# Optimization experiments

Measured on AMD Instinct MI355X. Metric: run time of the kernel, lower is better.

## Reference

```python
import jax, jax.numpy as jnp
import numpy as np

N = 4096      # num_nodes
D_IN = 768    # input_dim
HID = 512     # hidden_dim per head
D_OUT = 768   # output_dim
H = 4         # num_heads
ALPHA = 0.2   # LeakyReLU slope
NEG_BIG = -9e15


def _layer_norm(x, g, b, eps=1e-5):
    m = jnp.mean(x, axis=-1, keepdims=True)
    v = jnp.var(x, axis=-1, keepdims=True)
    return (x - m) * jax.lax.rsqrt(v + eps) * g + b


def _multihead_gat(h, mask, ew, W, a, concat):
    # h: [N, F_in], W: [H, F_in, O], a: [H, 2*O], mask/ew: [N, N]
    O = W.shape[-1]
    Wh = jnp.einsum('nf,hfo->hno', h, W)                      # [H, N, O]
    # e[h,i,j] = leakyrelu(a1.Wh[i] + a2.Wh[j]) -- equivalent to the
    # concat(Wh_i, Wh_j) @ a formulation, without the O(N^2 * 2O) tensor.
    s_src = jnp.einsum('hno,ho->hn', Wh, a[:, :O])            # [H, N]
    s_dst = jnp.einsum('hno,ho->hn', Wh, a[:, O:])            # [H, N]
    e = jax.nn.leaky_relu(s_src[:, :, None] + s_dst[:, None, :], negative_slope=ALPHA)
    att = jnp.where(mask[None], e, NEG_BIG)
    if ew is not None:
        att = att * ew[None]                                   # faithful: scale AFTER masking
    att = jax.nn.softmax(att, axis=-1)                         # dropout is identity at eval
    hp = jnp.einsum('hnm,hmo->hno', att, Wh)                   # [H, N, O]
    if concat:
        return jax.nn.elu(jnp.transpose(hp, (1, 0, 2)).reshape(h.shape[0], H * O))
    return jnp.mean(hp, axis=0)                                # concat=False: mean, no ELU


def setup_inputs() -> dict:
    key = jax.random.key(0)
    ks = jax.random.split(key, 10)
    return {
        'node_features': jax.random.normal(ks[0], (N, D_IN), jnp.float32),
        'adjacency': jax.random.randint(ks[1], (N, N), 0, 2, jnp.int32),
        'edge_weights': jax.random.uniform(ks[2], (N, N), jnp.float32),
        'W0': (jax.random.normal(ks[3], (H, D_IN, HID)) * 0.05).astype(jnp.float32),
        'a0': (jax.random.normal(ks[4], (H, 2 * HID)) * 0.05).astype(jnp.float32),
        'W1': (jax.random.normal(ks[5], (H, HID * H, D_OUT)) * 0.02).astype(jnp.float32),
        'a1': (jax.random.normal(ks[6], (H, 2 * D_OUT)) * 0.05).astype(jnp.float32),
        'rp0_w': (jax.random.normal(ks[7], (D_IN, HID * H)) * 0.02).astype(jnp.float32),
        'rp0_b': jnp.zeros((HID * H,), jnp.float32),
        'rp1_w': (jax.random.normal(ks[8], (HID * H, D_OUT)) * 0.02).astype(jnp.float32),
        'rp1_b': jnp.zeros((D_OUT,), jnp.float32),
        'ln0_g': jnp.ones((HID * H,), jnp.float32),
        'ln0_b': jnp.zeros((HID * H,), jnp.float32),
        'ln1_g': jnp.ones((D_OUT,), jnp.float32),
        'ln1_b': jnp.zeros((D_OUT,), jnp.float32),
    }


def reference(node_features, adjacency, edge_weights, W0, a0, W1, a1,
              rp0_w, rp0_b, rp1_w, rp1_b, ln0_g, ln0_b, ln1_g, ln1_b):
    n = node_features.shape[0]
    adj = adjacency.astype(jnp.float32) + jnp.eye(n, dtype=jnp.float32)  # add self-loops
    mask = adj > 0
    h = node_features
    # layer 0: concat heads -> [N, H*HID], residual projection, LN, ELU (dropout=identity)
    h1 = _multihead_gat(h, mask, edge_weights, W0, a0, concat=True)
    h1 = h1 + (h @ rp0_w + rp0_b)
    h1 = _layer_norm(h1, ln0_g, ln0_b)
    h1 = jax.nn.elu(h1)
    # layer 1 (last): mean over heads -> [N, D_OUT], residual projection, LN
    h2 = _multihead_gat(h1, mask, edge_weights, W1, a1, concat=False)
    h2 = h2 + (h1 @ rp1_w + rp1_b)
    h2 = _layer_norm(h2, ln1_g, ln1_b)
    return h2
```

## Files before the change

kernel.cpp:

```cpp
#include <hip/hip_runtime.h>


typedef unsigned short u16;
typedef unsigned char u8;
using short8  = __attribute__((ext_vector_type(8))) short;
using float4v = __attribute__((ext_vector_type(4))) float;
using int4v   = __attribute__((ext_vector_type(4))) int;
using int8v   = __attribute__((ext_vector_type(8))) int;

#define NN 4096
#define NHEADS 4

__device__ __forceinline__ u16 f2bf(float f) {
  union { float f; unsigned u; } v; v.f = f;
  unsigned u = v.u;
  return (u16)((u + 0x7FFFu + ((u >> 16) & 1u)) >> 16);
}
__device__ __forceinline__ float bf2f(u16 x) {
  union { unsigned u; float f; } v; v.u = ((unsigned)x) << 16; return v.f;
}
__device__ __forceinline__ unsigned pk_fp8x4(float a, float b, float c, float d) {
  int lo = __builtin_amdgcn_cvt_pk_fp8_f32(a, b, 0, false);
  return (unsigned)__builtin_amdgcn_cvt_pk_fp8_f32(c, d, lo, true);
}

__device__ __forceinline__ void async16(const void* g, void* l) {
  __builtin_amdgcn_global_load_lds(
      (const __attribute__((address_space(1))) unsigned int*)g,
      (__attribute__((address_space(3))) unsigned int*)l, 16, 0, 0);
}

__global__ __launch_bounds__(256) void cast_f32_bf16(const float* __restrict__ in,
                                                     u16* __restrict__ out, int n) {
  int i = blockIdx.x * 256 + threadIdx.x;
  if (i < n) out[i] = f2bf(in[i]);
}

__global__ __launch_bounds__(256) void transcast_f32(const float* __restrict__ in,
                                                     u16* __restrict__ out, int R, int C) {
  __shared__ float t[32][33];
  size_t zoff = (size_t)blockIdx.z * R * C;
  in += zoff; out += zoff;
  int c0 = blockIdx.x * 32, r0 = blockIdx.y * 32;
  int tx = threadIdx.x & 31, ty = threadIdx.x >> 5;
#pragma unroll
  for (int i = 0; i < 32; i += 8)
    t[ty + i][tx] = in[(size_t)(r0 + ty + i) * C + (c0 + tx)];
  __syncthreads();
#pragma unroll
  for (int i = 0; i < 32; i += 8)
    out[(size_t)(c0 + ty + i) * R + (r0 + tx)] = f2bf(t[tx][ty + i]);
}

__global__ __launch_bounds__(256) void wa_kernel(const float* __restrict__ W,
                                                 const float* __restrict__ a,
                                                 float* __restrict__ wa, int F, int O) {
  int gw = blockIdx.x * 4 + (threadIdx.x >> 6);
  int lane = threadIdx.x & 63;
  int total = 2 * NHEADS * F;
  if (gw >= total) return;
  int side = gw / (NHEADS * F);
  int rem = gw - side * NHEADS * F;
  int h = rem / F, f = rem - h * F;
  const float* wrow = W + ((size_t)h * F + f) * O;
  const float* av = a + (size_t)h * 2 * O + (size_t)side * O;
  float s = 0.f;
  for (int o = lane; o < O; o += 64) s += wrow[o] * av[o];
#pragma unroll
  for (int off = 32; off > 0; off >>= 1) s += __shfl_down(s, off);
  if (lane == 0) wa[gw] = s;
}

__global__ __launch_bounds__(256) void s8_kernel_f32(const float* __restrict__ X,
                                                     const float* __restrict__ wa,
                                                     float* __restrict__ sout, int F) {
  int n = blockIdx.x * 4 + (threadIdx.x >> 6);
  int lane = threadIdx.x & 63;
  const float* x = X + (size_t)n * F;
  float acc[8] = {};
  for (int f = lane; f < F; f += 64) {
    float xv = x[f];
#pragma unroll
    for (int k = 0; k < 8; k++) acc[k] += xv * wa[(size_t)k * F + f];
  }
#pragma unroll
  for (int k = 0; k < 8; k++) {
    float s = acc[k];
#pragma unroll
    for (int off = 32; off > 0; off >>= 1) s += __shfl_down(s, off);
    if (lane == 0) sout[(size_t)k * NN + n] = s;
  }
}

__global__ __launch_bounds__(256) void s8_kernel_bf16(const u16* __restrict__ X,
                                                      const float* __restrict__ wa,
                                                      float* __restrict__ sout, int F) {
  int n = blockIdx.x * 4 + (threadIdx.x >> 6);
  int lane = threadIdx.x & 63;
  const u16* x = X + (size_t)n * F;
  float acc[8] = {};
  for (int f = lane; f < F; f += 64) {
    float xv = bf2f(x[f]);
#pragma unroll
    for (int k = 0; k < 8; k++) acc[k] += xv * wa[(size_t)k * F + f];
  }
#pragma unroll
  for (int k = 0; k < 8; k++) {
    float s = acc[k];
#pragma unroll
    for (int off = 32; off > 0; off >>= 1) s += __shfl_down(s, off);
    if (lane == 0) sout[(size_t)k * NN + n] = s;
  }
}

template <int G>
__global__ __launch_bounds__(256) void pexp_g_kernel(const int* __restrict__ adj,
                                                     const float* __restrict__ ew,
                                                     const float* __restrict__ s,
                                                     u8* __restrict__ P,
                                                     float* __restrict__ L, int hb) {
  __shared__ float vbuf[G][NN];
  __shared__ float mred[G][4];
  __shared__ float lred[G][4];
  __shared__ float mrow[G];
  int i = blockIdx.x, tid = threadIdx.x;
  float sr[G], mx[G], lacc[G];
#pragma unroll
  for (int z = 0; z < G; z++) {
    sr[z] = s[(size_t)(hb + z) * NN + i];
    mx[z] = -3e38f;
    lacc[z] = 0.f;
  }
  const int4* arow = (const int4*)(adj + (size_t)i * NN);
  const float4* wrow = (const float4*)(ew + (size_t)i * NN);
  for (int jv = tid; jv < NN / 4; jv += 256) {
    int4 a = arow[jv];
    float4 w = wrow[jv];
    int j0 = jv * 4;
    float we[4]; we[0] = w.x; we[1] = w.y; we[2] = w.z; we[3] = w.w;
    bool m[4];
    m[0] = (a.x != 0) || (j0 + 0 == i);
    m[1] = (a.y != 0) || (j0 + 1 == i);
    m[2] = (a.z != 0) || (j0 + 2 == i);
    m[3] = (a.w != 0) || (j0 + 3 == i);
#pragma unroll
    for (int z = 0; z < G; z++) {
      const float4 sd4 = *(const float4*)(s + (size_t)(NHEADS + hb + z) * NN + j0);
      float sd[4]; sd[0] = sd4.x; sd[1] = sd4.y; sd[2] = sd4.z; sd[3] = sd4.w;
      float4 vv;
      float* vp = (float*)&vv;
#pragma unroll
      for (int k = 0; k < 4; k++) {
        float x = sr[z] + sd[k];
        float e = x > 0.f ? x : 0.2f * x;
        float v = (m[k] ? e : -9e15f) * we[k];
        vp[k] = v;
        mx[z] = fmaxf(mx[z], v);
      }
      *(float4*)(&vbuf[z][j0]) = vv;
    }
  }
#pragma unroll
  for (int z = 0; z < G; z++) {
    float r = mx[z];
#pragma unroll
    for (int off = 32; off > 0; off >>= 1) r = fmaxf(r, __shfl_down(r, off));
    if ((tid & 63) == 0) mred[z][tid >> 6] = r;
  }
  __syncthreads();
  if (tid < G)
    mrow[tid] = fmaxf(fmaxf(mred[tid][0], mred[tid][1]), fmaxf(mred[tid][2], mred[tid][3]));
  __syncthreads();
  float mv[G];
#pragma unroll
  for (int z = 0; z < G; z++) mv[z] = mrow[z];
  for (int jv = tid; jv < NN / 4; jv += 256) {
    int j0 = jv * 4;
#pragma unroll
    for (int z = 0; z < G; z++) {
      float4 vv = *(const float4*)(&vbuf[z][j0]);
      float p0 = __expf(vv.x - mv[z]);
      float p1 = __expf(vv.y - mv[z]);
      float p2 = __expf(vv.z - mv[z]);
      float p3 = __expf(vv.w - mv[z]);
      lacc[z] += (p0 + p1) + (p2 + p3);
      *(unsigned*)(P + ((size_t)z * NN + i) * NN + j0) = pk_fp8x4(p0, p1, p2, p3);
    }
  }
#pragma unroll
  for (int z = 0; z < G; z++) {
    float r = lacc[z];
#pragma unroll
    for (int off = 32; off > 0; off >>= 1) r += __shfl_down(r, off);
    if ((tid & 63) == 0) lred[z][tid >> 6] = r;
  }
  __syncthreads();
  if (tid < G)
    L[(size_t)(hb + tid) * NN + i] = lred[tid][0] + lred[tid][1] + lred[tid][2] + lred[tid][3];
}

__global__ __launch_bounds__(256) void gemm_proj(const u16* __restrict__ A,
                                                 const u16* __restrict__ Bt,
                                                 u8* __restrict__ F8T,
                                                 float* __restrict__ F32,
                                                 const float* __restrict__ bias,
                                                 int K, int split, int ldcF) {
  int row0 = blockIdx.x * 128;
  int col0 = blockIdx.y * 128;

  __shared__ u16 ldsA[128 * 64];
  __shared__ u16 ldsB[128 * 64];

  int tid = threadIdx.x;
  int wave = tid >> 6, lane = tid & 63;
  int wm = wave >> 1, wn = wave & 1;
  int lm = lane & 15, quad = lane >> 4;

  int sr = tid >> 3, sc = tid & 7;
  int scg = sc ^ (sr & 7);
  const u16* aPtr = A  + (size_t)(row0 + sr) * K + scg * 8;
  const u16* bPtr = Bt + (size_t)(col0 + sr) * K + scg * 8;
  u16* ldsAw = &ldsA[wave * 512];
  u16* ldsBw = &ldsB[wave * 512];
  const size_t rowStep = (size_t)32 * K;

  float4v acc[4][4] = {};

  for (int k0 = 0; k0 < K; k0 += 64) {
    __syncthreads();
#pragma unroll
    for (int b = 0; b < 4; b++) {
      async16(aPtr + k0 + b * rowStep, ldsAw + b * 2048);
      async16(bPtr + k0 + b * rowStep, ldsBw + b * 2048);
    }
    __syncthreads();
    short8 af[4][2], bf[4][2];
#pragma unroll
    for (int s = 0; s < 4; s++) {
      int ra = wm * 64 + s * 16 + lm;
      int rb = wn * 64 + s * 16 + lm;
      int swa = ra & 7, swb = rb & 7;
      af[s][0] = *(const short8*)(&ldsA[ra * 64 + ((quad ^ swa) * 8)]);
      af[s][1] = *(const short8*)(&ldsA[ra * 64 + (((4 + quad) ^ swa) * 8)]);
      bf[s][0] = *(const short8*)(&ldsB[rb * 64 + ((quad ^ swb) * 8)]);
      bf[s][1] = *(const short8*)(&ldsB[rb * 64 + (((4 + quad) ^ swb) * 8)]);
    }
#pragma unroll
    for (int i = 0; i < 4; i++)
#pragma unroll
      for (int j = 0; j < 4; j++) {
        acc[i][j] = __builtin_amdgcn_mfma_f32_16x16x32_bf16(af[i][0], bf[j][0], acc[i][j], 0, 0, 0);
        acc[i][j] = __builtin_amdgcn_mfma_f32_16x16x32_bf16(af[i][1], bf[j][1], acc[i][j], 0, 0, 0);
      }
  }

  if (col0 < split) {
#pragma unroll
    for (int i = 0; i < 4; i++) {
#pragma unroll
      for (int j = 0; j < 4; j++) {
        int grow0 = row0 + wm * 64 + i * 16 + (lane >> 4) * 4;
        int gcol = col0 + wn * 64 + j * 16 + lm;
        unsigned pk = pk_fp8x4(acc[i][j][0], acc[i][j][1], acc[i][j][2], acc[i][j][3]);
        *(unsigned*)&F8T[(size_t)gcol * NN + grow0] = pk;
      }
    }
  } else {
#pragma unroll
    for (int i = 0; i < 4; i++) {
#pragma unroll
      for (int j = 0; j < 4; j++) {
#pragma unroll
        for (int r = 0; r < 4; r++) {
          int grow = row0 + wm * 64 + i * 16 + (lane >> 4) * 4 + r;
          int gcol = col0 + wn * 64 + j * 16 + lm - split;
          F32[(size_t)grow * ldcF + gcol] = acc[i][j][r] + bias[gcol];
        }
      }
    }
  }
}

template <int MODE>
__global__ __launch_bounds__(256) void gemm_mx(const u8* __restrict__ A,
                                               const u8* __restrict__ Bt,
                                               float* __restrict__ Cout,
                                               int ldc, int coloff_base, int coloff_step,
                                               size_t bStride, size_t cStride) {
  constexpr int K = NN;
  int h = blockIdx.z;
  const u8* Ab = A + (size_t)h * ((size_t)NN * NN);
  const u8* Bb = Bt + (size_t)h * bStride;
  int row0 = blockIdx.x * 128;
  int col0 = blockIdx.y * 128;
  int coloff = coloff_base + h * coloff_step;

  __shared__ u8 ldsA[128 * 128];
  __shared__ u8 ldsB[128 * 128];

  int tid = threadIdx.x;
  int wave = tid >> 6, lane = tid & 63;
  int wm = wave >> 1, wn = wave & 1;
  int lm = lane & 15, quad = lane >> 4;

  int sr = tid >> 3, sc = tid & 7;
  int scg = sc ^ (sr & 7);
  const u8* aPtr = Ab + (size_t)(row0 + sr) * K + scg * 16;
  const u8* bPtr = Bb + (size_t)(col0 + sr) * K + scg * 16;
  u8* ldsAw = &ldsA[wave * 1024];
  u8* ldsBw = &ldsB[wave * 1024];
  const size_t rowStep = (size_t)32 * K;

  float4v acc[4][4] = {};

  for (int k0 = 0; k0 < K; k0 += 128) {
    __syncthreads();
#pragma unroll
    for (int b = 0; b < 4; b++) {
      async16(aPtr + k0 + b * rowStep, ldsAw + b * 4096);
      async16(bPtr + k0 + b * rowStep, ldsBw + b * 4096);
    }
    __syncthreads();
    int8v a32[4], b32[4];
#pragma unroll
    for (int s = 0; s < 4; s++) {
      int ra = wm * 64 + s * 16 + lm;
      int rb = wn * 64 + s * 16 + lm;
      int swa = ra & 7, swb = rb & 7;
      int4v alo = *(const int4v*)(&ldsA[ra * 128 + (((2 * quad) ^ swa) * 16)]);
      int4v ahi = *(const int4v*)(&ldsA[ra * 128 + (((2 * quad + 1) ^ swa) * 16)]);
      int4v blo = *(const int4v*)(&ldsB[rb * 128 + (((2 * quad) ^ swb) * 16)]);
      int4v bhi = *(const int4v*)(&ldsB[rb * 128 + (((2 * quad + 1) ^ swb) * 16)]);
      a32[s][0] = alo[0]; a32[s][1] = alo[1]; a32[s][2] = alo[2]; a32[s][3] = alo[3];
      a32[s][4] = ahi[0]; a32[s][5] = ahi[1]; a32[s][6] = ahi[2]; a32[s][7] = ahi[3];
      b32[s][0] = blo[0]; b32[s][1] = blo[1]; b32[s][2] = blo[2]; b32[s][3] = blo[3];
      b32[s][4] = bhi[0]; b32[s][5] = bhi[1]; b32[s][6] = bhi[2]; b32[s][7] = bhi[3];
    }
#pragma unroll
    for (int i = 0; i < 4; i++)
#pragma unroll
      for (int j = 0; j < 4; j++)
        acc[i][j] = __builtin_amdgcn_mfma_scale_f32_16x16x128_f8f6f4(
            a32[i], b32[j], acc[i][j], 0, 0, 0, 127, 0, 127);
  }

#pragma unroll
  for (int i = 0; i < 4; i++) {
#pragma unroll
    for (int j = 0; j < 4; j++) {
#pragma unroll
      for (int r = 0; r < 4; r++) {
        int grow = row0 + wm * 64 + i * 16 + quad * 4 + r;
        int gcol = col0 + wn * 64 + j * 16 + lm;
        float v = acc[i][j][r];
        if constexpr (MODE == 2) {
          Cout[(size_t)grow * ldc + coloff + gcol] = v;
        } else {
          Cout[(size_t)h * cStride + (size_t)grow * ldc + gcol] = v;
        }
      }
    }
  }
}

__global__ __launch_bounds__(256) void ln0_kernel(const float* __restrict__ accin,
                                                  const float* __restrict__ rp,
                                                  const float* __restrict__ Lsum,
                                                  const float* __restrict__ g,
                                                  const float* __restrict__ b,
                                                  u16* __restrict__ h1b) {
  const int C = 2048;
  int n = blockIdx.x, tid = threadIdx.x;
  __shared__ float xs[2048];
  __shared__ float red[2][4];
  __shared__ float mrs[2];
  float linv[NHEADS];
#pragma unroll
  for (int h = 0; h < NHEADS; h++) linv[h] = 1.0f / Lsum[(size_t)h * NN + n];
  float sum = 0.f, sq = 0.f;
  const float* ar = accin + (size_t)n * C;
  const float* rr = rp + (size_t)n * C;
  for (int c = tid; c < C; c += 256) {
    float v = ar[c] * linv[c >> 9];
    v = v > 0.f ? v : (__expf(v) - 1.f);
    float x = v + rr[c];
    xs[c] = x; sum += x; sq += x * x;
  }
#pragma unroll
  for (int off = 32; off > 0; off >>= 1) { sum += __shfl_down(sum, off); sq += __shfl_down(sq, off); }
  if ((tid & 63) == 0) { red[0][tid >> 6] = sum; red[1][tid >> 6] = sq; }
  __syncthreads();
  if (tid == 0) {
    float s = red[0][0] + red[0][1] + red[0][2] + red[0][3];
    float q = red[1][0] + red[1][1] + red[1][2] + red[1][3];
    float mean = s / C, var = q / C - mean * mean;
    mrs[0] = mean; mrs[1] = rsqrtf(var + 1e-5f);
  }
  __syncthreads();
  float mean = mrs[0], rstd = mrs[1];
  for (int c = tid; c < C; c += 256) {
    float y = (xs[c] - mean) * rstd * g[c] + b[c];
    float z = y > 0.f ? y : (__expf(y) - 1.f);
    h1b[(size_t)n * C + c] = f2bf(z);
  }
}

__global__ __launch_bounds__(256) void ln1_kernel(const float* __restrict__ hp1,
                                                  const float* __restrict__ rp1,
                                                  const float* __restrict__ Lsum,
                                                  const float* __restrict__ g,
                                                  const float* __restrict__ b,
                                                  float* __restrict__ out) {
  const int C = 768;
  int n = blockIdx.x, tid = threadIdx.x;
  __shared__ float xs[768];
  __shared__ float red[2][4];
  __shared__ float mrs[2];
  float linv[NHEADS];
#pragma unroll
  for (int h = 0; h < NHEADS; h++) linv[h] = 0.25f / Lsum[(size_t)h * NN + n];
  float sum = 0.f, sq = 0.f;
  for (int c = tid; c < C; c += 256) {
    float x = hp1[((size_t)0 * NN + n) * C + c] * linv[0] +
              hp1[((size_t)1 * NN + n) * C + c] * linv[1] +
              hp1[((size_t)2 * NN + n) * C + c] * linv[2] +
              hp1[((size_t)3 * NN + n) * C + c] * linv[3];
    x += rp1[(size_t)n * C + c];
    xs[c] = x; sum += x; sq += x * x;
  }
#pragma unroll
  for (int off = 32; off > 0; off >>= 1) { sum += __shfl_down(sum, off); sq += __shfl_down(sq, off); }
  if ((tid & 63) == 0) { red[0][tid >> 6] = sum; red[1][tid >> 6] = sq; }
  __syncthreads();
  if (tid == 0) {
    float s = red[0][0] + red[0][1] + red[0][2] + red[0][3];
    float q = red[1][0] + red[1][1] + red[1][2] + red[1][3];
    float mean = s / C, var = q / C - mean * mean;
    mrs[0] = mean; mrs[1] = rsqrtf(var + 1e-5f);
  }
  __syncthreads();
  float mean = mrs[0], rstd = mrs[1];
  for (int c = tid; c < C; c += 256)
    out[(size_t)n * C + c] = (xs[c] - mean) * rstd * g[c] + b[c];
}

extern "C" void kernel_launch(void* const* d_in, const int* in_sizes, int n_in,
                              void* d_out, int out_size, void* d_ws, size_t ws_size,
                              hipStream_t stream) {
  (void)in_sizes; (void)n_in; (void)out_size;
  const float* X    = (const float*)d_in[0];
  const int*   adj  = (const int*)d_in[1];
  const float* ew   = (const float*)d_in[2];
  const float* W0   = (const float*)d_in[3];
  const float* a0   = (const float*)d_in[4];
  const float* W1   = (const float*)d_in[5];
  const float* a1   = (const float*)d_in[6];
  const float* rp0w = (const float*)d_in[7];
  const float* rp0b = (const float*)d_in[8];
  const float* rp1w = (const float*)d_in[9];
  const float* rp1b = (const float*)d_in[10];
  const float* ln0g = (const float*)d_in[11];
  const float* ln0b = (const float*)d_in[12];
  const float* ln1g = (const float*)d_in[13];
  const float* ln1b = (const float*)d_in[14];
  float* out = (float*)d_out;
  char* wsb = (char*)d_ws;

  constexpr size_t OFF_XBF   = 0;
  constexpr size_t OFF_W0T   = 6291456;
  constexpr size_t OFF_RP0WT = 9437184;
  constexpr size_t OFF_W1T   = 12582912;
  constexpr size_t OFF_RP1WT = 25165824;
  constexpr size_t OFF_WA0   = 28311552;
  constexpr size_t OFF_WA1   = 28336128;
  constexpr size_t OFF_S0    = 28401664;
  constexpr size_t OFF_S1    = 28532736;
  constexpr size_t OFF_L0    = 28664320;
  constexpr size_t OFF_L1    = 28729856;
  constexpr size_t OFF_H1B   = 28795392;
  constexpr size_t D         = 45572608;
  constexpr size_t PD        = D + 50331648;
  constexpr size_t PN        = (size_t)NN * NN;
  constexpr size_t OFF_HP1   = PD + 4 * PN;

  u16*   XBF   = (u16*)(wsb + OFF_XBF);
  u16*   W0T   = (u16*)(wsb + OFF_W0T);
  u16*   RP0WT = (u16*)(wsb + OFF_RP0WT);
  u16*   W1T   = (u16*)(wsb + OFF_W1T);
  u16*   RP1WT = (u16*)(wsb + OFF_RP1WT);
  float* WA0   = (float*)(wsb + OFF_WA0);
  float* WA1   = (float*)(wsb + OFF_WA1);
  float* S0    = (float*)(wsb + OFF_S0);
  float* S1    = (float*)(wsb + OFF_S1);
  float* L0    = (float*)(wsb + OFF_L0);
  float* L1    = (float*)(wsb + OFF_L1);
  u16*   H1B   = (u16*)(wsb + OFF_H1B);
  u8*    WH0T  = (u8*)(wsb + D);
  float* RP0   = (float*)(wsb + D + 16777216);
  u8*    WH1T  = (u8*)(wsb + D);
  float* RP1   = (float*)(wsb + D + 25165824);
  u8*    P     = (u8*)(wsb + PD);
  float* HP1   = (float*)(wsb + OFF_HP1);
  float* ACC0  = (float*)(wsb + OFF_HP1);

  const int G = (ws_size >= OFF_HP1 + 50331648) ? 4 : 1;

  cast_f32_bf16<<<dim3((NN * 768 + 255) / 256), 256, 0, stream>>>(X, XBF, NN * 768);
  transcast_f32<<<dim3(16, 24, 4), 256, 0, stream>>>(W0, W0T, 768, 512);
  transcast_f32<<<dim3(24, 64, 4), 256, 0, stream>>>(W1, W1T, 2048, 768);
  transcast_f32<<<dim3(64, 24, 1), 256, 0, stream>>>(rp0w, RP0WT, 768, 2048);
  transcast_f32<<<dim3(24, 64, 1), 256, 0, stream>>>(rp1w, RP1WT, 2048, 768);

  wa_kernel<<<dim3(2 * NHEADS * 768 / 4), 256, 0, stream>>>(W0, a0, WA0, 768, 512);
  s8_kernel_f32<<<dim3(NN / 4), 256, 0, stream>>>(X, WA0, S0, 768);

  gemm_proj<<<dim3(32, 32), 256, 0, stream>>>(XBF, W0T, WH0T, RP0, rp0b, 768, 2048, 2048);

  for (int g = 0; g < NHEADS; g += G) {
    if (G == 4) pexp_g_kernel<4><<<dim3(NN), 256, 0, stream>>>(adj, ew, S0, P, L0, g);
    else        pexp_g_kernel<1><<<dim3(NN), 256, 0, stream>>>(adj, ew, S0, P, L0, g);
    gemm_mx<2><<<dim3(32, 4, G), 256, 0, stream>>>(P, WH0T + (size_t)g * 512 * NN,
        ACC0, 2048, g * 512, 512, (size_t)512 * NN, 0);
  }
  ln0_kernel<<<dim3(NN), 256, 0, stream>>>(ACC0, RP0, L0, ln0g, ln0b, H1B);

  wa_kernel<<<dim3(2 * NHEADS * 2048 / 4), 256, 0, stream>>>(W1, a1, WA1, 2048, 768);
  s8_kernel_bf16<<<dim3(NN / 4), 256, 0, stream>>>(H1B, WA1, S1, 2048);

  gemm_proj<<<dim3(32, 30), 256, 0, stream>>>(H1B, W1T, WH1T, RP1, rp1b, 2048, 3072, 768);

  for (int g = 0; g < NHEADS; g += G) {
    if (G == 4) pexp_g_kernel<4><<<dim3(NN), 256, 0, stream>>>(adj, ew, S1, P, L1, g);
    else        pexp_g_kernel<1><<<dim3(NN), 256, 0, stream>>>(adj, ew, S1, P, L1, g);
    gemm_mx<3><<<dim3(32, 6, G), 256, 0, stream>>>(P, WH1T + (size_t)g * 768 * NN,
        HP1 + (size_t)g * NN * 768, 768, 0, 0, (size_t)768 * NN, (size_t)NN * 768);
  }
  ln1_kernel<<<dim3(NN), 256, 0, stream>>>(HP1, RP1, L1, ln1g, ln1b, out);
}
```

Before: 685.0 us.

## Pack adjacency into bitmask and make masked softmax single-pass with score upper bound

Adds a pre-pass that packs the int32 adjacency matrix into a 64-bit-per-64-column bitmask, so each attention-probability kernel reads 1/32 of the mask bytes. It also computes the per-head maximum of destination scores and uses max(0, s_src + max s_dst) as a row-wise upper bound on the logits. That turns the two-pass softmax, which staged logits in a large LDS buffer and did a block max reduction, into one pass that writes fp8 probabilities and row sums directly. This cuts global traffic and LDS use, which should allow more resident blocks. The bound only holds when edge weights lie in [0,1], and a loose bound could push small probabilities into fp8 underflow.

Result: faster. 642.2 us (-6.2%).

```diff
diff --git a/kernel.cpp b/kernel.cpp
--- a/kernel.cpp
+++ b/kernel.cpp
@@ -3,6 +3,7 @@
 
 typedef unsigned short u16;
 typedef unsigned char u8;
+typedef unsigned long long u64;
 using short8  = __attribute__((ext_vector_type(8))) short;
 using float4v = __attribute__((ext_vector_type(4))) float;
 using int4v   = __attribute__((ext_vector_type(4))) int;
@@ -34,6 +35,15 @@
                                                      u16* __restrict__ out, int n) {
   int i = blockIdx.x * 256 + threadIdx.x;
   if (i < n) out[i] = f2bf(in[i]);
+}
+
+__global__ __launch_bounds__(256) void adj2bits(const int* __restrict__ adj,
+                                                u64* __restrict__ bits) {
+  size_t gw = (size_t)blockIdx.x * 4 + (threadIdx.x >> 6);
+  int lane = threadIdx.x & 63;
+  int v = adj[gw * 64 + lane];
+  u64 b = __ballot(v != 0);
+  if (lane == 0) bits[gw] = b;
 }
 
 __global__ __launch_bounds__(256) void transcast_f32(const float* __restrict__ in,
@@ -113,78 +123,62 @@
   }
 }
 
+__global__ __launch_bounds__(256) void sdmax_kernel(const float* __restrict__ s,
+                                                    float* __restrict__ out) {
+  int h = blockIdx.x, tid = threadIdx.x;
+  const float* sd = s + (size_t)(NHEADS + h) * NN;
+  float m = -3e38f;
+  for (int i = tid; i < NN; i += 256) m = fmaxf(m, sd[i]);
+  __shared__ float red[4];
+#pragma unroll
+  for (int off = 32; off > 0; off >>= 1) m = fmaxf(m, __shfl_down(m, off));
+  if ((tid & 63) == 0) red[tid >> 6] = m;
+  __syncthreads();
+  if (tid == 0) out[h] = fmaxf(fmaxf(red[0], red[1]), fmaxf(red[2], red[3]));
+}
+
 template <int G>
-__global__ __launch_bounds__(256) void pexp_g_kernel(const int* __restrict__ adj,
+__global__ __launch_bounds__(256) void pexp_g_kernel(const u64* __restrict__ mb,
                                                      const float* __restrict__ ew,
                                                      const float* __restrict__ s,
+                                                     const float* __restrict__ sdmax,
                                                      u8* __restrict__ P,
                                                      float* __restrict__ L, int hb) {
-  __shared__ float vbuf[G][NN];
-  __shared__ float mred[G][4];
+  __shared__ u64 mrow[64];
   __shared__ float lred[G][4];
-  __shared__ float mrow[G];
   int i = blockIdx.x, tid = threadIdx.x;
-  float sr[G], mx[G], lacc[G];
+  if (tid < 64) mrow[tid] = mb[(size_t)i * 64 + tid];
+  float sr[G], mp[G], lacc[G];
 #pragma unroll
   for (int z = 0; z < G; z++) {
     sr[z] = s[(size_t)(hb + z) * NN + i];
-    mx[z] = -3e38f;
+    mp[z] = fmaxf(0.0f, sr[z] + sdmax[hb + z]);
     lacc[z] = 0.f;
   }
-  const int4* arow = (const int4*)(adj + (size_t)i * NN);
   const float4* wrow = (const float4*)(ew + (size_t)i * NN);
+  __syncthreads();
   for (int jv = tid; jv < NN / 4; jv += 256) {
-    int4 a = arow[jv];
     float4 w = wrow[jv];
     int j0 = jv * 4;
+    u64 mw = mrow[jv >> 4] >> (j0 & 63);
     float we[4]; we[0] = w.x; we[1] = w.y; we[2] = w.z; we[3] = w.w;
     bool m[4];
-    m[0] = (a.x != 0) || (j0 + 0 == i);
-    m[1] = (a.y != 0) || (j0 + 1 == i);
-    m[2] = (a.z != 0) || (j0 + 2 == i);
-    m[3] = (a.w != 0) || (j0 + 3 == i);
+#pragma unroll
+    for (int k = 0; k < 4; k++) m[k] = ((mw >> k) & 1ull) || (j0 + k == i);
 #pragma unroll
     for (int z = 0; z < G; z++) {
       const float4 sd4 = *(const float4*)(s + (size_t)(NHEADS + hb + z) * NN + j0);
       float sd[4]; sd[0] = sd4.x; sd[1] = sd4.y; sd[2] = sd4.z; sd[3] = sd4.w;
-      float4 vv;
-      float* vp = (float*)&vv;
+      float p[4];
 #pragma unroll
       for (int k = 0; k < 4; k++) {
         float x = sr[z] + sd[k];
         float e = x > 0.f ? x : 0.2f * x;
         float v = (m[k] ? e : -9e15f) * we[k];
-        vp[k] = v;
-        mx[z] = fmaxf(mx[z], v);
+        p[k] = __expf(v - mp[z]);
+        lacc[z] += p[k];
       }
-      *(float4*)(&vbuf[z][j0]) = vv;
-    }
-  }
-#pragma unroll
-  for (int z = 0; z < G; z++) {
-    float r = mx[z];
-#pragma unroll
-    for (int off = 32; off > 0; off >>= 1) r = fmaxf(r, __shfl_down(r, off));
-    if ((tid & 63) == 0) mred[z][tid >> 6] = r;
-  }
-  __syncthreads();
-  if (tid < G)
-    mrow[tid] = fmaxf(fmaxf(mred[tid][0], mred[tid][1]), fmaxf(mred[tid][2], mred[tid][3]));
-  __syncthreads();
-  float mv[G];
-#pragma unroll
-  for (int z = 0; z < G; z++) mv[z] = mrow[z];
-  for (int jv = tid; jv < NN / 4; jv += 256) {
-    int j0 = jv * 4;
-#pragma unroll
-    for (int z = 0; z < G; z++) {
-      float4 vv = *(const float4*)(&vbuf[z][j0]);
-      float p0 = __expf(vv.x - mv[z]);
-      float p1 = __expf(vv.y - mv[z]);
-      float p2 = __expf(vv.z - mv[z]);
-      float p3 = __expf(vv.w - mv[z]);
-      lacc[z] += (p0 + p1) + (p2 + p3);
-      *(unsigned*)(P + ((size_t)z * NN + i) * NN + j0) = pk_fp8x4(p0, p1, p2, p3);
+      *(unsigned*)(P + ((size_t)z * NN + i) * NN + j0) = pk_fp8x4(p[0], p[1], p[2], p[3]);
     }
   }
 #pragma unroll
@@ -482,6 +476,9 @@
   constexpr size_t PD        = D + 50331648;
   constexpr size_t PN        = (size_t)NN * NN;
   constexpr size_t OFF_HP1   = PD + 4 * PN;
+  constexpr size_t OFF_MASK  = 213344768;
+  constexpr size_t OFF_SM0   = 215441920;
+  constexpr size_t OFF_SM1   = 215442176;
 
   u16*   XBF   = (u16*)(wsb + OFF_XBF);
   u16*   W0T   = (u16*)(wsb + OFF_W0T);
@@ -502,9 +499,13 @@
   u8*    P     = (u8*)(wsb + PD);
   float* HP1   = (float*)(wsb + OFF_HP1);
   float* ACC0  = (float*)(wsb + OFF_HP1);
+  u64*   MASK  = (u64*)(wsb + OFF_MASK);
+  float* SM0   = (float*)(wsb + OFF_SM0);
+  float* SM1   = (float*)(wsb + OFF_SM1);
 
   const int G = (ws_size >= OFF_HP1 + 50331648) ? 4 : 1;
 
+  adj2bits<<<dim3(65536), 256, 0, stream>>>(adj, MASK);
   cast_f32_bf16<<<dim3((NN * 768 + 255) / 256), 256, 0, stream>>>(X, XBF, NN * 768);
   transcast_f32<<<dim3(16, 24, 4), 256, 0, stream>>>(W0, W0T, 768, 512);
   transcast_f32<<<dim3(24, 64, 4), 256, 0, stream>>>(W1, W1T, 2048, 768);
@@ -513,12 +514,13 @@
 
   wa_kernel<<<dim3(2 * NHEADS * 768 / 4), 256, 0, stream>>>(W0, a0, WA0, 768, 512);
   s8_kernel_f32<<<dim3(NN / 4), 256, 0, stream>>>(X, WA0, S0, 768);
+  sdmax_kernel<<<dim3(NHEADS), 256, 0, stream>>>(S0, SM0);
 
   gemm_proj<<<dim3(32, 32), 256, 0, stream>>>(XBF, W0T, WH0T, RP0, rp0b, 768, 2048, 2048);
 
   for (int g = 0; g < NHEADS; g += G) {
-    if (G == 4) pexp_g_kernel<4><<<dim3(NN), 256, 0, stream>>>(adj, ew, S0, P, L0, g);
-    else        pexp_g_kernel<1><<<dim3(NN), 256, 0, stream>>>(adj, ew, S0, P, L0, g);
+    if (G == 4) pexp_g_kernel<4><<<dim3(NN), 256, 0, stream>>>(MASK, ew, S0, SM0, P, L0, g);
+    else        pexp_g_kernel<1><<<dim3(NN), 256, 0, stream>>>(MASK, ew, S0, SM0, P, L0, g);
     gemm_mx<2><<<dim3(32, 4, G), 256, 0, stream>>>(P, WH0T + (size_t)g * 512 * NN,
         ACC0, 2048, g * 512, 512, (size_t)512 * NN, 0);
   }
@@ -526,12 +528,13 @@
 
   wa_kernel<<<dim3(2 * NHEADS * 2048 / 4), 256, 0, stream>>>(W1, a1, WA1, 2048, 768);
   s8_kernel_bf16<<<dim3(NN / 4), 256, 0, stream>>>(H1B, WA1, S1, 2048);
+  sdmax_kernel<<<dim3(NHEADS), 256, 0, stream>>>(S1, SM1);
 
   gemm_proj<<<dim3(32, 30), 256, 0, stream>>>(H1B, W1T, WH1T, RP1, rp1b, 2048, 3072, 768);
 
   for (int g = 0; g < NHEADS; g += G) {
-    if (G == 4) pexp_g_kernel<4><<<dim3(NN), 256, 0, stream>>>(adj, ew, S1, P, L1, g);
-    else        pexp_g_kernel<1><<<dim3(NN), 256, 0, stream>>>(adj, ew, S1, P, L1, g);
+    if (G == 4) pexp_g_kernel<4><<<dim3(NN), 256, 0, stream>>>(MASK, ew, S1, SM1, P, L1, g);
+    else        pexp_g_kernel<1><<<dim3(NN), 256, 0, stream>>>(MASK, ew, S1, SM1, P, L1, g);
     gemm_mx<3><<<dim3(32, 6, G), 256, 0, stream>>>(P, WH1T + (size_t)g * 768 * NN,
         HP1 + (size_t)g * NN * 768, 768, 0, 0, (size_t)768 * NN, (size_t)NN * 768);
   }
```
